# Kernel optimization log

Measured on AMD Instinct MI355X. Metric: run time of the kernel, lower is better.

Reference implementation:

```python
import jax, jax.numpy as jnp
import numpy as np
from jax import lax

B, T, Dm = 2, 2048, 2048
H, DK, DV = 16, 128, 128      # num heads, head_k_dim, head_v_dim
KW = 4                         # conv kernel size
CONV_DIM = 2 * H * DK + H * DV
EPS = 1e-6


def setup_inputs() -> dict:
    key = jax.random.key(0)
    ks = jax.random.split(key, 10)
    s = 0.02
    return {
        "x": jax.random.normal(ks[0], (B, T, Dm), dtype=jnp.float32),
        "w_qkv": jax.random.normal(ks[1], (CONV_DIM, Dm), dtype=jnp.float32) * s,
        "conv_w": jax.random.normal(ks[2], (CONV_DIM, KW), dtype=jnp.float32) * 0.2,
        "w_z": jax.random.normal(ks[3], (H * DV, Dm), dtype=jnp.float32) * s,
        "w_b": jax.random.normal(ks[4], (H, Dm), dtype=jnp.float32) * s,
        "w_a": jax.random.normal(ks[5], (H, Dm), dtype=jnp.float32) * s,
        "dt_bias": jnp.ones((H,), dtype=jnp.float32),
        "A_log": jnp.log(jax.random.uniform(ks[6], (H,), minval=0.5, maxval=16.0)).astype(jnp.float32),
        "norm_w": jnp.ones((DV,), dtype=jnp.float32),
        "w_out": jax.random.normal(ks[7], (Dm, H * DV), dtype=jnp.float32) * s,
    }


def _l2norm(u):
    return u * lax.rsqrt(jnp.sum(u * u, axis=-1, keepdims=True) + EPS)


def reference(x, w_qkv, conv_w, w_z, w_b, w_a, dt_bias, A_log, norm_w, w_out):
    # qkv projection: [B,T,CONV_DIM]
    mixed = jnp.einsum('btd,cd->btc', x, w_qkv)
    # causal depthwise conv + SiLU
    xc = mixed.transpose(0, 2, 1)                       # [B,C,T]
    y = lax.conv_general_dilated(
        xc, conv_w[:, None, :], window_strides=(1,),
        padding=[(KW - 1, 0)], feature_group_count=CONV_DIM)
    y = jax.nn.silu(y).transpose(0, 2, 1)               # [B,T,C]

    q = _l2norm(y[..., :H * DK].reshape(B, T, H, DK))
    k = _l2norm(y[..., H * DK:2 * H * DK].reshape(B, T, H, DK))
    v = y[..., 2 * H * DK:].reshape(B, T, H, DV)

    # per-head gates
    beta = jax.nn.sigmoid(jnp.einsum('btd,hd->bth', x, w_b))               # [B,T,H]
    g = -jnp.exp(A_log) * jax.nn.softplus(jnp.einsum('btd,hd->bth', x, w_a) + dt_bias)
    decay = jnp.exp(g)                                                     # [B,T,H]

    # time-major for scan
    qT = q.transpose(1, 0, 2, 3)
    kT = k.transpose(1, 0, 2, 3)
    vT = v.transpose(1, 0, 2, 3)
    dT = decay.transpose(1, 0, 2)
    bT = beta.transpose(1, 0, 2)

    def step(S, inp):
        q_t, k_t, v_t, d_t, b_t = inp
        S = S * d_t[..., None, None]                                       # [B,H,DK,DV]
        kv = jnp.einsum('bhk,bhkv->bhv', k_t, S)
        S = S + jnp.einsum('bhk,bhv->bhkv', k_t, (v_t - kv) * b_t[..., None])
        o_t = jnp.einsum('bhk,bhkv->bhv', q_t, S)
        return S, o_t

    S0 = jnp.zeros((B, H, DK, DV), dtype=x.dtype)
    _, o = lax.scan(step, S0, (qT, kT, vT, dT, bT))                        # [T,B,H,DV]
    o = o.transpose(1, 0, 2, 3)                                            # [B,T,H,DV]

    # gated RMSNorm per head, gate = silu(z)
    z = jnp.einsum('btd,ed->bte', x, w_z).reshape(B, T, H, DV)
    on = o * lax.rsqrt(jnp.mean(o * o, axis=-1, keepdims=True) + EPS)
    on = on * norm_w * jax.nn.silu(z)

    return jnp.einsum('bte,de->btd', on.reshape(B, T, H * DV), w_out)
```

## Files before the change

kernel.cpp:

```cpp
#include <hip/hip_runtime.h>
#include <hip/hip_bf16.h>

#define B_   2
#define T_   2048
#define DM   2048
#define H_   16
#define DK_  128
#define DV_  128
#define CDIM 6144
#define EPSF 1e-6f
#define CGRP 16
#define CROWS 16

typedef __hip_bfloat16 bf16;
typedef _Float16 f16;
typedef short bf16x8 __attribute__((ext_vector_type(8)));
typedef _Float16 f16x8 __attribute__((ext_vector_type(8)));
typedef float f32x4 __attribute__((ext_vector_type(4)));
typedef float f32x2 __attribute__((ext_vector_type(2)));

#define FLAG_OFF   0
#define DT_OFF     1024
#define AL_OFF     2048
#define NW_OFF     4096
#define CW_OFF     8192
#define WBF_OFF    131072
#define WAF_OFF    262144
#define BETA_OFF   393216
#define DEC_OFF    655360
#define XH_OFF     1048576
#define XL_OFF     17825792
#define WQH_OFF    34603008
#define WZCAT_OFF  59768832
#define MIX_OFF    101711872
#define WOUT_OFF   202375168
#define Z_OFF      210763776
#define Y_OFF      1048576
#define O_OFF      101711872
#define ONH_OFF    1048576

__device__ inline float bf2f(unsigned int u) {
  union { unsigned int i; float f; } v; v.i = u << 16; return v.f;
}
__device__ inline void up8(uint4 p, float* d) {
  d[0] = bf2f(p.x & 0xffffu); d[1] = bf2f(p.x >> 16);
  d[2] = bf2f(p.y & 0xffffu); d[3] = bf2f(p.y >> 16);
  d[4] = bf2f(p.z & 0xffffu); d[5] = bf2f(p.z >> 16);
  d[6] = bf2f(p.w & 0xffffu); d[7] = bf2f(p.w >> 16);
}
__device__ inline void up8h(uint4 p, float* d) {
  union { unsigned int i; _Float16 h[2]; } c;
  c.i = p.x; d[0] = (float)c.h[0]; d[1] = (float)c.h[1];
  c.i = p.y; d[2] = (float)c.h[0]; d[3] = (float)c.h[1];
  c.i = p.z; d[4] = (float)c.h[0]; d[5] = (float)c.h[1];
  c.i = p.w; d[6] = (float)c.h[0]; d[7] = (float)c.h[1];
}
__device__ inline void gl2lds16(const void* g, void* lds) {
  __builtin_amdgcn_global_load_lds(
      (const __attribute__((address_space(1))) unsigned int*)g,
      (__attribute__((address_space(3))) unsigned int*)lds, 16, 0, 0);
}
__device__ inline void stage_fence() {
  asm volatile("s_waitcnt vmcnt(0) lgkmcnt(0)" ::: "memory");
}

__device__ inline f32x2 pkfma(f32x2 a, f32x2 b, f32x2 c) {
  return __builtin_elementwise_fma(a, b, c);
}

template <int CTRL>
__device__ inline float radd(float v) {
  int t = __builtin_amdgcn_update_dpp(0, __float_as_int(v), CTRL, 0xF, 0xF, true);
  return v + __int_as_float(t);
}
__device__ inline float row_sum16(float v) {
  v = radd<0xB1>(v);
  v = radd<0x4E>(v);
  v = radd<0x141>(v);
  v = radd<0x140>(v);
  return v;
}

__global__ __launch_bounds__(256) void detect_dtype(
    const unsigned short* __restrict__ xh, int* __restrict__ flag) {
  __shared__ int cnt;
  if (threadIdx.x == 0) cnt = 0;
  __syncthreads();
  int c = 0;
  for (int i = threadIdx.x; i < 8192; i += 256) {
    unsigned int e = (xh[i] >> 7) & 0xFFu;
    if (e > 140u) c++;
  }
  atomicAdd(&cnt, c);
  __syncthreads();
  if (threadIdx.x == 0) *flag = (cnt > 512) ? 1 : 0;
}

__device__ inline void canon_seg(const void* in, char* d0, char* d1, int n,
                                 int mode, int f32in, int i) {
  if (i >= n) return;
  float v[8];
  if (f32in) {
    const float* f = (const float*)in;
    *(float4*)(v)     = *(const float4*)(f + i);
    *(float4*)(v + 4) = *(const float4*)(f + i + 4);
  } else {
    up8(*(const uint4*)((const bf16*)in + i), v);
  }
  if (mode == 0) {
    *(float4*)((float*)d0 + i)     = *(const float4*)(v);
    *(float4*)((float*)d0 + i + 4) = *(const float4*)(v + 4);
  } else if (mode == 3) {
    f16 t[8];
#pragma unroll
    for (int j = 0; j < 8; j++) t[j] = (f16)v[j];
    *(uint4*)((f16*)d0 + i) = *(const uint4*)t;
  } else {
    f16 th[8], tl[8];
#pragma unroll
    for (int j = 0; j < 8; j++) {
      th[j] = (f16)v[j];
      tl[j] = (f16)(v[j] - (float)th[j]);
    }
    *(uint4*)((f16*)d0 + i) = *(const uint4*)th;
    *(uint4*)((f16*)d1 + i) = *(const uint4*)tl;
  }
}

__global__ __launch_bounds__(256) void canon_all(
    const void* x, const void* wqkv, const void* cw, const void* wz,
    const void* wb, const void* wa, const void* dt, const void* al,
    const void* nw, const void* wout, char* ws, const int* __restrict__ flag) {
  const int bk = blockIdx.x;
  const int f32in = *flag;
  if (bk < 1)
    canon_seg(dt, ws + DT_OFF, 0, 16, 0, f32in, (bk - 0) * 2048 + threadIdx.x * 8);
  else if (bk < 2)
    canon_seg(al, ws + AL_OFF, 0, 16, 0, f32in, (bk - 1) * 2048 + threadIdx.x * 8);
  else if (bk < 3)
    canon_seg(nw, ws + NW_OFF, 0, 128, 0, f32in, (bk - 2) * 2048 + threadIdx.x * 8);
  else if (bk < 15)
    canon_seg(cw, ws + CW_OFF, 0, CDIM * 4, 0, f32in, (bk - 3) * 2048 + threadIdx.x * 8);
  else if (bk < 31)
    canon_seg(wb, ws + WBF_OFF, 0, H_ * DM, 0, f32in, (bk - 15) * 2048 + threadIdx.x * 8);
  else if (bk < 47)
    canon_seg(wa, ws + WAF_OFF, 0, H_ * DM, 0, f32in, (bk - 31) * 2048 + threadIdx.x * 8);
  else if (bk < 4143)
    canon_seg(x, ws + XH_OFF, ws + XL_OFF, B_ * T_ * DM, 4, f32in,
              (bk - 47) * 2048 + threadIdx.x * 8);
  else if (bk < 10287)
    canon_seg(wqkv, ws + WQH_OFF, 0, CDIM * DM, 3, f32in,
              (bk - 4143) * 2048 + threadIdx.x * 8);
  else if (bk < 12335)
    canon_seg(wz, ws + WZCAT_OFF, 0, H_ * DV_ * DM, 3, f32in,
              (bk - 10287) * 2048 + threadIdx.x * 8);
  else
    canon_seg(wout, ws + WOUT_OFF, 0, DM * H_ * DV_, 3, f32in,
              (bk - 12335) * 2048 + threadIdx.x * 8);
}

template <int OMODE>
__global__ __launch_bounds__(256) void gemm_f16(
    const f16* __restrict__ Ah, const f16* __restrict__ Bm,
    void* __restrict__ C, int M, int N, int K, const int* __restrict__ flag) {
  __shared__ __align__(16) f16 sAh[128 * 32];
  __shared__ __align__(16) f16 sB[128 * 32];
  const int tid  = threadIdx.x;
  const int wave = tid >> 6;
  const int lane = tid & 63;
  const int m0 = blockIdx.y * 128;
  const int n0 = blockIdx.x * 128;
  const int wm = (wave >> 1) * 64;
  const int wn = (wave & 1) * 64;
  const int lrow = lane & 15;
  const int kq   = lane >> 4;

  f32x4 acc[4][4];
#pragma unroll
  for (int i = 0; i < 4; i++)
#pragma unroll
    for (int j = 0; j < 4; j++) acc[i][j] = (f32x4){0.f, 0.f, 0.f, 0.f};

  const int row0 = tid >> 2;
  const int cb   = (tid & 3) * 8;
  const size_t aoff = (size_t)(m0 + row0) * K + cb;
  const size_t boff = (size_t)(n0 + row0) * K + cb;

  for (int k0 = 0; k0 < K; k0 += 32) {
    gl2lds16(Ah + aoff + k0,                  sAh + wave * 512);
    gl2lds16(Ah + aoff + k0 + (size_t)64 * K, sAh + 2048 + wave * 512);
    gl2lds16(Bm + boff + k0,                  sB + wave * 512);
    gl2lds16(Bm + boff + k0 + (size_t)64 * K, sB + 2048 + wave * 512);
    stage_fence();
    __syncthreads();

    f16x8 afh[4], bfr[4];
#pragma unroll
    for (int i = 0; i < 4; i++) {
      afh[i] = *(const f16x8*)(sAh + (wm + i * 16 + lrow) * 32 + kq * 8);
      bfr[i] = *(const f16x8*)(sB + (wn + i * 16 + lrow) * 32 + kq * 8);
    }
#pragma unroll
    for (int i = 0; i < 4; i++)
#pragma unroll
      for (int j = 0; j < 4; j++)
        acc[i][j] = __builtin_amdgcn_mfma_f32_16x16x32_f16(afh[i], bfr[j], acc[i][j], 0, 0, 0);
    __syncthreads();
  }

  const int f32o = (OMODE == 0) ? 1 : ((OMODE == 2) ? *flag : 0);
#pragma unroll
  for (int i = 0; i < 4; i++) {
    const int r0 = m0 + wm + i * 16 + kq * 4;
#pragma unroll
    for (int j = 0; j < 4; j++) {
      const int c = n0 + wn + j * 16 + lrow;
#pragma unroll
      for (int r = 0; r < 4; r++) {
        const size_t idx = (size_t)(r0 + r) * N + c;
        if (f32o) ((float*)C)[idx] = acc[i][j][r];
        else      ((bf16*)C)[idx] = __float2bfloat16(acc[i][j][r]);
      }
    }
  }
}

__global__ __launch_bounds__(256) void gemm_qkvz(
    const f16* __restrict__ Ah, const f16* __restrict__ Bm,
    float* __restrict__ Cmix, bf16* __restrict__ Cz, int M, int K) {
  __shared__ __align__(16) f16 sAh[128 * 32];
  __shared__ __align__(16) f16 sB[128 * 32];
  const int tid  = threadIdx.x;
  const int wave = tid >> 6;
  const int lane = tid & 63;
  const int m0 = blockIdx.y * 128;
  const int n0 = blockIdx.x * 128;
  const int wm = (wave >> 1) * 64;
  const int wn = (wave & 1) * 64;
  const int lrow = lane & 15;
  const int kq   = lane >> 4;

  f32x4 acc[4][4];
#pragma unroll
  for (int i = 0; i < 4; i++)
#pragma unroll
    for (int j = 0; j < 4; j++) acc[i][j] = (f32x4){0.f, 0.f, 0.f, 0.f};

  const int row0 = tid >> 2;
  const int cb   = (tid & 3) * 8;
  const size_t aoff = (size_t)(m0 + row0) * K + cb;
  const size_t boff = (size_t)(n0 + row0) * K + cb;

  for (int k0 = 0; k0 < K; k0 += 32) {
    gl2lds16(Ah + aoff + k0,                  sAh + wave * 512);
    gl2lds16(Ah + aoff + k0 + (size_t)64 * K, sAh + 2048 + wave * 512);
    gl2lds16(Bm + boff + k0,                  sB + wave * 512);
    gl2lds16(Bm + boff + k0 + (size_t)64 * K, sB + 2048 + wave * 512);
    stage_fence();
    __syncthreads();

    f16x8 afh[4], bfr[4];
#pragma unroll
    for (int i = 0; i < 4; i++) {
      afh[i] = *(const f16x8*)(sAh + (wm + i * 16 + lrow) * 32 + kq * 8);
      bfr[i] = *(const f16x8*)(sB + (wn + i * 16 + lrow) * 32 + kq * 8);
    }
#pragma unroll
    for (int i = 0; i < 4; i++)
#pragma unroll
      for (int j = 0; j < 4; j++)
        acc[i][j] = __builtin_amdgcn_mfma_f32_16x16x32_f16(afh[i], bfr[j], acc[i][j], 0, 0, 0);
    __syncthreads();
  }

  const bool zout = (n0 >= CDIM);
#pragma unroll
  for (int i = 0; i < 4; i++) {
    const int r0 = m0 + wm + i * 16 + kq * 4;
#pragma unroll
    for (int j = 0; j < 4; j++) {
      const int c = n0 + wn + j * 16 + lrow;
#pragma unroll
      for (int r = 0; r < 4; r++) {
        if (zout)
          Cz[(size_t)(r0 + r) * (H_ * DV_) + (c - CDIM)] =
              __float2bfloat16(acc[i][j][r]);
        else
          Cmix[(size_t)(r0 + r) * CDIM + c] = acc[i][j][r];
      }
    }
  }
}

__global__ __launch_bounds__(128) void conv_silu_norm(
    const float* __restrict__ mixed, const float* __restrict__ convw,
    float* __restrict__ y) {
  const int g  = blockIdx.x;
  const int n0 = blockIdx.y * CROWS;
  const int c  = g * 128 + threadIdx.x;

  const float4 w = *(const float4*)(convw + (size_t)c * 4);
  __shared__ float red[2];

  float x1, x2, x3;
  {
    const int t0 = n0 & (T_ - 1);
    const float* mc = mixed + (size_t)n0 * CDIM + c;
    x1 = (t0 >= 1) ? mc[-CDIM]     : 0.f;
    x2 = (t0 >= 2) ? mc[-2 * CDIM] : 0.f;
    x3 = (t0 >= 3) ? mc[-3 * CDIM] : 0.f;
  }
  float x0 = mixed[(size_t)n0 * CDIM + c];

#pragma unroll 4
  for (int i = 0; i < CROWS; i++) {
    const int n = n0 + i;
    float xn = 0.f;
    if (i + 1 < CROWS) xn = mixed[(size_t)(n + 1) * CDIM + c];

    float a = x0 * w.w + x1 * w.z + x2 * w.y + x3 * w.x;
    float s = a / (1.f + expf(-a));

    if (g < 32) {
      float ss = s * s;
#pragma unroll
      for (int o = 32; o > 0; o >>= 1) ss += __shfl_xor(ss, o);
      if ((threadIdx.x & 63) == 0) red[threadIdx.x >> 6] = ss;
      __syncthreads();
      s *= rsqrtf(red[0] + red[1] + EPSF);
      __syncthreads();
    }
    y[(size_t)n * CDIM + c] = s;

    x3 = x2; x2 = x1; x1 = x0; x0 = xn;
  }
}

__global__ __launch_bounds__(256) void gates_kernel(
    const f16* __restrict__ xh, const f16* __restrict__ xl,
    const float* __restrict__ w_b, const float* __restrict__ w_a,
    const float* __restrict__ dtb, const float* __restrict__ alog,
    float* __restrict__ beta, float* __restrict__ decay) {
  const int n = blockIdx.x, tid = threadIdx.x;
  __shared__ float xs[DM];
  __shared__ float red[32][8];
  {
    uint4 ph = ((const uint4*)(xh + (size_t)n * DM))[tid];
    uint4 pl = ((const uint4*)(xl + (size_t)n * DM))[tid];
    float h[8], l[8]; up8h(ph, h); up8h(pl, l);
    const int b = tid * 8;
#pragma unroll
    for (int j = 0; j < 8; j++) xs[b + j] = h[j] + l[j];
  }
  __syncthreads();
  const int hh = tid >> 3, part = tid & 7;
  const float* wrow =
      (hh < 16 ? w_b + (size_t)hh * DM : w_a + (size_t)(hh - 16) * DM) + part * 256;
  const float* xp = xs + part * 256;
  float sum = 0.f;
#pragma unroll 4
  for (int i = 0; i < 256; i += 4) {
    float4 p = *(const float4*)(wrow + i);
    sum += xp[i + 0] * p.x + xp[i + 1] * p.y + xp[i + 2] * p.z + xp[i + 3] * p.w;
  }
  red[hh][part] = sum;
  __syncthreads();
  if (tid < 32) {
    float d = 0.f;
#pragma unroll
    for (int p = 0; p < 8; p++) d += red[tid][p];
    if (tid < 16) {
      beta[(size_t)n * H_ + tid] = 1.f / (1.f + expf(-d));
    } else {
      const int h = tid - 16;
      float u = d + dtb[h];
      float sp = (u > 20.f) ? u : log1pf(expf(u));
      decay[(size_t)n * H_ + h] = expf(-expf(alog[h]) * sp);
    }
  }
}

__global__ __launch_bounds__(256, 1) void scan_kernel(
    const float* __restrict__ y, const float* __restrict__ beta,
    const float* __restrict__ decay, float* __restrict__ o) {
  const int vb = blockIdx.x, h = blockIdx.y, b = blockIdx.z;
  const int tid = threadIdx.x;
  const int kg = tid & 15;
  const int vl = tid >> 4;

  __shared__ __align__(16) float sq[2][CGRP][128];
  __shared__ __align__(16) float sk[2][CGRP][128];
  __shared__ __align__(16) float sv[2][CGRP][16];
  __shared__ float sd[2][CGRP];
  __shared__ float sb[2][CGRP];

  const size_t rowbase = (size_t)b * T_ * CDIM;
  const int qoff = h * 128;
  const int koff = 2048 + h * 128;
  const int voff = 4096 + h * 128 + vb * 16;
  const float* bb = beta + (size_t)b * T_ * H_ + h;
  const float* db = decay + (size_t)b * T_ * H_ + h;
  float* ob = o + (size_t)b * T_ * (H_ * DV_) + h * 128 + vb * 16 + vl;

  const int ls = tid >> 4;
  const int lj = tid & 15;

  f32x2 S2[4];
#pragma unroll
  for (int j = 0; j < 4; j++) S2[j] = (f32x2){0.f, 0.f};

  float4 ga0, ga1, gb0, gb1, gv4;
  float gdd = 0.f, gbt = 0.f;

#define STAGE_ISSUE(t0)                                                      \
  {                                                                          \
    const float* r = y + rowbase + (size_t)((t0) + ls) * CDIM;               \
    ga0 = *(const float4*)(r + qoff + lj * 4);                               \
    ga1 = *(const float4*)(r + qoff + 64 + lj * 4);                          \
    gb0 = *(const float4*)(r + koff + lj * 4);                               \
    gb1 = *(const float4*)(r + koff + 64 + lj * 4);                          \
    if (tid < 64)                                                            \
      gv4 = *(const float4*)(y + rowbase + (size_t)((t0) + (tid >> 2)) * CDIM\
                             + voff + (tid & 3) * 4);                        \
    if (tid < 16) gdd = db[(size_t)((t0) + tid) * H_];                       \
    else if (tid < 32) gbt = bb[(size_t)((t0) + tid - 16) * H_];             \
  }

#define STAGE_WRITE(buf)                                                     \
  {                                                                          \
    *(float4*)&sq[buf][ls][lj * 4]      = ga0;                               \
    *(float4*)&sq[buf][ls][64 + lj * 4] = ga1;                               \
    *(float4*)&sk[buf][ls][lj * 4]      = gb0;                               \
    *(float4*)&sk[buf][ls][64 + lj * 4] = gb1;                               \
    if (tid < 64) *(float4*)&sv[buf][tid >> 2][(tid & 3) * 4] = gv4;         \
    if (tid < 16) sd[buf][tid] = gdd;                                        \
    else if (tid < 32) sb[buf][tid - 16] = gbt;                              \
  }

#define CVT2(dst, a, bfour)                                                  \
  {                                                                          \
    float4 _a = (a), _b = (bfour);                                           \
    dst[0] = (f32x2){_a.x, _a.y}; dst[1] = (f32x2){_a.z, _a.w};              \
    dst[2] = (f32x2){_b.x, _b.y}; dst[3] = (f32x2){_b.z, _b.w};              \
  }

#define READ_PAIR(buf, r, Q1, K1, Q2, K2, P)                                 \
  {                                                                          \
    CVT2(Q1, *(const float4*)&sq[buf][2*(r)][kg * 4],                        \
             *(const float4*)&sq[buf][2*(r)][64 + kg * 4]);                  \
    CVT2(K1, *(const float4*)&sk[buf][2*(r)][kg * 4],                        \
             *(const float4*)&sk[buf][2*(r)][64 + kg * 4]);                  \
    CVT2(Q2, *(const float4*)&sq[buf][2*(r)+1][kg * 4],                      \
             *(const float4*)&sq[buf][2*(r)+1][64 + kg * 4]);                \
    CVT2(K2, *(const float4*)&sk[buf][2*(r)+1][kg * 4],                      \
             *(const float4*)&sk[buf][2*(r)+1][64 + kg * 4]);                \
    P##v1 = sv[buf][2*(r)][vl];   P##d1 = sd[buf][2*(r)];   P##b1 = sb[buf][2*(r)];   \
    P##v2 = sv[buf][2*(r)+1][vl]; P##d2 = sd[buf][2*(r)+1]; P##b2 = sb[buf][2*(r)+1]; \
  }

  STAGE_ISSUE(0);
  STAGE_WRITE(0);
  __syncthreads();

  f32x2 q1[4], k1[4], q2[4], k2[4];
  f32x2 nq1[4], nk1[4], nq2[4], nk2[4];
  float cv1, cd1, cb1, cv2, cd2, cb2;
  float nv1, nd1, nb1, nv2, nd2, nb2;
  float pp[CGRP];
  READ_PAIR(0, 0, q1, k1, q2, k2, c);

  const int NGRP = T_ / CGRP;
  const int NRND = CGRP / 2;
  for (int g = 0; g < NGRP; g++) {
    const int cbuf = g & 1, nbuf = cbuf ^ 1;
    const bool more = (g + 1 < NGRP);
    if (more) STAGE_ISSUE((g + 1) * CGRP);
#pragma unroll
    for (int r = 0; r < NRND; r++) {
      if (r < NRND - 1) READ_PAIR(cbuf, r + 1, nq1, nk1, nq2, nk2, n);
      f32x2 ma = pkfma(k2[1], k1[1], k2[0] * k1[0]);
      f32x2 mb = pkfma(k2[3], k1[3], k2[2] * k1[2]);
      f32x2 mv = ma + mb;
      float mm = row_sum16(mv.x + mv.y);
      f32x2 ca = pkfma(S2[1], k1[1], S2[0] * k1[0]);
      f32x2 cb_ = pkfma(S2[3], k1[3], S2[2] * k1[2]);
      f32x2 cvv = ca + cb_;
      f32x2 wa = pkfma(S2[1], k2[1], S2[0] * k2[0]);
      f32x2 wb = pkfma(S2[3], k2[3], S2[2] * k2[2]);
      f32x2 wvv = wa + wb;
      float c1s = row_sum16(cvv.x + cvv.y);
      float w2s = row_sum16(wvv.x + wvv.y);
      const float u1 = fmaf(-cd1, c1s, cv1) * cb1;
      const float kv2 = fmaf(mm, u1, cd1 * w2s);
      const float u2 = fmaf(-cd2, kv2, cv2) * cb2;
      {
        const f32x2 dv = (f32x2){cd1, cd1}, uv = (f32x2){u1, u1};
#pragma unroll
        for (int j = 0; j < 4; j++) S2[j] = pkfma(dv, S2[j], k1[j] * uv);
        f32x2 pa = pkfma(S2[1], q1[1], S2[0] * q1[0]);
        f32x2 pb = pkfma(S2[3], q1[3], S2[2] * q1[2]);
        f32x2 pv = pa + pb;
        pp[2 * r] = pv.x + pv.y;
      }
      {
        const f32x2 dv = (f32x2){cd2, cd2}, uv = (f32x2){u2, u2};
#pragma unroll
        for (int j = 0; j < 4; j++) S2[j] = pkfma(dv, S2[j], k2[j] * uv);
        f32x2 pa = pkfma(S2[1], q2[1], S2[0] * q2[0]);
        f32x2 pb = pkfma(S2[3], q2[3], S2[2] * q2[2]);
        f32x2 pv = pa + pb;
        pp[2 * r + 1] = pv.x + pv.y;
      }
      if (r < NRND - 1) {
#pragma unroll
        for (int j = 0; j < 4; j++) {
          q1[j] = nq1[j]; k1[j] = nk1[j]; q2[j] = nq2[j]; k2[j] = nk2[j];
        }
        cv1 = nv1; cd1 = nd1; cb1 = nb1; cv2 = nv2; cd2 = nd2; cb2 = nb2;
      }
    }
#pragma unroll
    for (int s = 0; s < CGRP; s++) pp[s] = row_sum16(pp[s]);
    if (kg == 0) {
#pragma unroll
      for (int s = 0; s < CGRP; s++)
        ob[(size_t)(g * CGRP + s) * (H_ * DV_)] = pp[s];
    }
    if (more) {
      STAGE_WRITE(nbuf);
      __syncthreads();
      READ_PAIR(nbuf, 0, q1, k1, q2, k2, c);
    }
  }
#undef STAGE_ISSUE
#undef STAGE_WRITE
#undef READ_PAIR
#undef CVT2
}

__global__ __launch_bounds__(128) void norm_gate(
    const float* __restrict__ o, const bf16* __restrict__ z,
    const float* __restrict__ norm_w, f16* __restrict__ on_h) {
  const int n = blockIdx.x, v = threadIdx.x;
  const float nw = norm_w[v];
  __shared__ float red[2];
  const size_t base = (size_t)n * (H_ * DV_) + v;

  float ov = o[base];
  float zv = __bfloat162float(z[base]);
#pragma unroll 4
  for (int h = 0; h < H_; h++) {
    float ovn = 0.f, zvn = 0.f;
    if (h + 1 < H_) {
      ovn = o[base + (h + 1) * 128];
      zvn = __bfloat162float(z[base + (h + 1) * 128]);
    }
    float ss = ov * ov;
#pragma unroll
    for (int w = 32; w > 0; w >>= 1) ss += __shfl_xor(ss, w);
    if ((v & 63) == 0) red[v >> 6] = ss;
    __syncthreads();
    const float ms = (red[0] + red[1]) * (1.f / 128.f);
    __syncthreads();
    const float res = ov * rsqrtf(ms + EPSF) * nw * (zv / (1.f + expf(-zv)));
    on_h[base + h * 128] = (f16)res;
    ov = ovn; zv = zvn;
  }
}

extern "C" void kernel_launch(void* const* d_in, const int* in_sizes, int n_in,
                              void* d_out, int out_size, void* d_ws, size_t ws_size,
                              hipStream_t stream) {
  const int NT = B_ * T_;
  char* ws = (char*)d_ws;
  int*   flag   = (int*)(ws + FLAG_OFF);
  float* dt_f   = (float*)(ws + DT_OFF);
  float* al_f   = (float*)(ws + AL_OFF);
  float* nw_f   = (float*)(ws + NW_OFF);
  float* cw_f   = (float*)(ws + CW_OFF);
  float* wb_f   = (float*)(ws + WBF_OFF);
  float* wa_f   = (float*)(ws + WAF_OFF);
  float* betab  = (float*)(ws + BETA_OFF);
  float* decayb = (float*)(ws + DEC_OFF);
  f16*   x_hi   = (f16*)(ws + XH_OFF);
  f16*   x_lo   = (f16*)(ws + XL_OFF);
  f16*   wqz_h  = (f16*)(ws + WQH_OFF);
  float* mixed  = (float*)(ws + MIX_OFF);
  f16*   wout_h = (f16*)(ws + WOUT_OFF);
  bf16*  z      = (bf16*)(ws + Z_OFF);
  float* y      = (float*)(ws + Y_OFF);
  float* o      = (float*)(ws + O_OFF);
  f16*   on_h   = (f16*)(ws + ONH_OFF);

  detect_dtype<<<1, 256, 0, stream>>>((const unsigned short*)d_in[0], flag);

  canon_all<<<14383, 256, 0, stream>>>(
      d_in[0], d_in[1], d_in[2], d_in[3], d_in[4], d_in[5], d_in[6], d_in[7],
      d_in[8], d_in[9], ws, flag);

  gates_kernel<<<NT, 256, 0, stream>>>(x_hi, x_lo, wb_f, wa_f, dt_f, al_f,
                                       betab, decayb);
  gemm_qkvz<<<dim3((CDIM + H_ * DV_) / 128, NT / 128), 256, 0, stream>>>(
      x_hi, wqz_h, mixed, z, NT, DM);
  conv_silu_norm<<<dim3(CDIM / 128, NT / CROWS), 128, 0, stream>>>(
      mixed, cw_f, y);
  scan_kernel<<<dim3(DV_ / 16, H_, B_), 256, 0, stream>>>(y, betab, decayb, o);
  norm_gate<<<NT, 128, 0, stream>>>(o, z, nw_f, on_h);
  gemm_f16<2><<<dim3(DM / 128, NT / 128), 256, 0, stream>>>(
      on_h, wout_h, d_out, NT, DM, H_ * DV_, flag);
}
```

Before: 867.6 us.

## Store qkv projection output in fp16 and swizzle GEMM blocks across XCDs

The intermediate 'mixed' buffer written by the qkvz GEMM and read by the conv kernel is stored as fp16 instead of fp32, halving that round-trip traffic. Both GEMM kernels also remap block indices so that consecutive tiles are spread in chunks across the eight XCDs, aiming for better L2 locality. The fp16 storage loses precision in the pre-conv activations, and the remap assumes the block count is divisible by 8.

Result: no change. 852.7 us (-1.7%).

```diff
diff --git a/kernel.cpp b/kernel.cpp
--- a/kernel.cpp
+++ b/kernel.cpp
@@ -66,6 +66,16 @@
 
 __device__ inline f32x2 pkfma(f32x2 a, f32x2 b, f32x2 c) {
   return __builtin_elementwise_fma(a, b, c);
+}
+
+__device__ inline void xcd_swz(int& bx, int& by) {
+  const int gx = gridDim.x;
+  const int nwg = gx * gridDim.y;
+  const int flat = by * gx + bx;
+  const int q = nwg >> 3;
+  const int wg = (flat & 7) * q + (flat >> 3);
+  bx = wg % gx;
+  by = wg / gx;
 }
 
 template <int CTRL>
@@ -168,8 +178,10 @@
   const int tid  = threadIdx.x;
   const int wave = tid >> 6;
   const int lane = tid & 63;
-  const int m0 = blockIdx.y * 128;
-  const int n0 = blockIdx.x * 128;
+  int bx = blockIdx.x, by = blockIdx.y;
+  xcd_swz(bx, by);
+  const int m0 = by * 128;
+  const int n0 = bx * 128;
   const int wm = (wave >> 1) * 64;
   const int wn = (wave & 1) * 64;
   const int lrow = lane & 15;
@@ -227,14 +239,16 @@
 
 __global__ __launch_bounds__(256) void gemm_qkvz(
     const f16* __restrict__ Ah, const f16* __restrict__ Bm,
-    float* __restrict__ Cmix, bf16* __restrict__ Cz, int M, int K) {
+    f16* __restrict__ Cmix, bf16* __restrict__ Cz, int M, int K) {
   __shared__ __align__(16) f16 sAh[128 * 32];
   __shared__ __align__(16) f16 sB[128 * 32];
   const int tid  = threadIdx.x;
   const int wave = tid >> 6;
   const int lane = tid & 63;
-  const int m0 = blockIdx.y * 128;
-  const int n0 = blockIdx.x * 128;
+  int bx = blockIdx.x, by = blockIdx.y;
+  xcd_swz(bx, by);
+  const int m0 = by * 128;
+  const int n0 = bx * 128;
   const int wm = (wave >> 1) * 64;
   const int wn = (wave & 1) * 64;
   const int lrow = lane & 15;
@@ -286,14 +300,14 @@
           Cz[(size_t)(r0 + r) * (H_ * DV_) + (c - CDIM)] =
               __float2bfloat16(acc[i][j][r]);
         else
-          Cmix[(size_t)(r0 + r) * CDIM + c] = acc[i][j][r];
+          Cmix[(size_t)(r0 + r) * CDIM + c] = (f16)acc[i][j][r];
       }
     }
   }
 }
 
 __global__ __launch_bounds__(128) void conv_silu_norm(
-    const float* __restrict__ mixed, const float* __restrict__ convw,
+    const f16* __restrict__ mixed, const float* __restrict__ convw,
     float* __restrict__ y) {
   const int g  = blockIdx.x;
   const int n0 = blockIdx.y * CROWS;
@@ -305,18 +319,18 @@
   float x1, x2, x3;
   {
     const int t0 = n0 & (T_ - 1);
-    const float* mc = mixed + (size_t)n0 * CDIM + c;
-    x1 = (t0 >= 1) ? mc[-CDIM]     : 0.f;
-    x2 = (t0 >= 2) ? mc[-2 * CDIM] : 0.f;
-    x3 = (t0 >= 3) ? mc[-3 * CDIM] : 0.f;
-  }
-  float x0 = mixed[(size_t)n0 * CDIM + c];
+    const f16* mc = mixed + (size_t)n0 * CDIM + c;
+    x1 = (t0 >= 1) ? (float)mc[-CDIM]     : 0.f;
+    x2 = (t0 >= 2) ? (float)mc[-2 * CDIM] : 0.f;
+    x3 = (t0 >= 3) ? (float)mc[-3 * CDIM] : 0.f;
+  }
+  float x0 = (float)mixed[(size_t)n0 * CDIM + c];
 
 #pragma unroll 4
   for (int i = 0; i < CROWS; i++) {
     const int n = n0 + i;
     float xn = 0.f;
-    if (i + 1 < CROWS) xn = mixed[(size_t)(n + 1) * CDIM + c];
+    if (i + 1 < CROWS) xn = (float)mixed[(size_t)(n + 1) * CDIM + c];
 
     float a = x0 * w.w + x1 * w.z + x2 * w.y + x3 * w.x;
     float s = a / (1.f + expf(-a));
@@ -585,7 +599,7 @@
   f16*   x_hi   = (f16*)(ws + XH_OFF);
   f16*   x_lo   = (f16*)(ws + XL_OFF);
   f16*   wqz_h  = (f16*)(ws + WQH_OFF);
-  float* mixed  = (float*)(ws + MIX_OFF);
+  f16*   mixed  = (f16*)(ws + MIX_OFF);
   f16*   wout_h = (f16*)(ws + WOUT_OFF);
   bf16*  z      = (bf16*)(ws + Z_OFF);
   float* y      = (float*)(ws + Y_OFF);
```
